# Performance work log

Hardware: AMD Instinct MI355X
Metric: run time of the kernel (lower is better)

## Reference

```python
import jax, jax.numpy as jnp
import numpy as np
import math

# tcnn HashGrid config (hard-coded in the torch module)
N_LEVELS = 16
N_FEATS = 2
LOG2_T = 19
T = 1 << LOG2_T            # 524288 entries per level
BASE_RES = 16
PER_LEVEL_SCALE = 1.4472692012786865
PRIMES = (1, 2654435761, 805459861)  # tcnn coherent spatial hash primes
N_POINTS = 1 << 20

# 8 trilinear corner offsets, [8, 3]
_OFFSETS = np.stack(np.meshgrid(*([np.arange(2)] * 3), indexing='ij'), -1).reshape(8, 3)


def _level_scale_res(level):
    # tcnn: grid_scale = base * s^l - 1 ; resolution = ceil(grid_scale) + 1
    scale = BASE_RES * (PER_LEVEL_SCALE ** level) - 1.0
    res = int(math.ceil(scale)) + 1
    return scale, res


def hashgrid_encode(coords, table):
    """coords: [..., 3] in [0,1]; table: [N_LEVELS, T, N_FEATS].
    Returns [..., N_LEVELS * N_FEATS]."""
    lead_shape = coords.shape[:-1]
    x = coords.reshape(-1, 3)                         # [N, 3]
    offs_i = jnp.asarray(_OFFSETS, dtype=jnp.uint32)  # [8, 3]
    offs_f = jnp.asarray(_OFFSETS, dtype=coords.dtype)
    feats = []
    for l in range(N_LEVELS):
        scale, res = _level_scale_res(l)
        pos = x * jnp.asarray(scale, x.dtype) + 0.5   # [N, 3]
        pf = jnp.floor(pos)
        w = pos - pf                                   # trilinear weights in [0,1)
        grid = pf.astype(jnp.uint32)                  # [N, 3]
        c = grid[None, :, :] + offs_i[:, None, :]     # [8, N, 3] corner coords
        if res ** 3 <= T:
            # dense (non-hashed) indexing for coarse levels
            cc = jnp.minimum(c, jnp.uint32(res - 1)).astype(jnp.int32)
            idx = cc[..., 0] + cc[..., 1] * res + cc[..., 2] * (res * res)
        else:
            # spatial hash: XOR of per-dim prime products, mod 2^19
            h = (c[..., 0] * jnp.uint32(PRIMES[0])
                 ^ c[..., 1] * jnp.uint32(PRIMES[1])
                 ^ c[..., 2] * jnp.uint32(PRIMES[2]))
            idx = (h & jnp.uint32(T - 1)).astype(jnp.int32)
        v = table[l][idx]                             # [8, N, F] gathered features
        # per-corner trilinear weight: prod over dims of (w or 1-w)
        wc = jnp.prod(jnp.where(offs_f[:, None, :] == 1.0, w[None], 1.0 - w[None]), axis=-1)  # [8, N]
        feats.append(jnp.einsum('kn,knf->nf', wc, v))  # [N, F]
    out = jnp.concatenate(feats, axis=-1)             # [N, 32]
    return out.reshape(*lead_shape, N_LEVELS * N_FEATS)


def setup_inputs() -> dict:
    key = jax.random.key(0)
    k1, k2 = jax.random.split(key)
    coords = jax.random.uniform(k1, (N_POINTS, 3), dtype=jnp.float32)
    # tcnn initializes hash table uniform in [-1e-4, 1e-4]
    table = jax.random.uniform(k2, (N_LEVELS, T, N_FEATS), dtype=jnp.float32,
                               minval=-1e-4, maxval=1e-4)
    return {"coords": coords, "table": table}


def reference(coords, table):
    return hashgrid_encode(coords, table)
```

## Files before the change

kernel.cpp:

```cpp
#include <hip/hip_runtime.h>
#include <math.h>

#define TBL   (1u << 19)
#define TMASK (TBL - 1u)
#define PRIME1 2654435761u
#define PRIME2 805459861u

#define N_DENSE  5u
#define N_HASH   11u

typedef float v2f __attribute__((ext_vector_type(2)));
typedef float v4f __attribute__((ext_vector_type(4)));

struct LevelParams {
    float    scale[16];
    unsigned res[16];
    unsigned dense[16];
};

__device__ __forceinline__ void corner_indices(
    float x, float y, float z, float s, unsigned res, unsigned dense,
    unsigned idx[8], float* wx, float* wy, float* wz)
{
    float px = __fadd_rn(__fmul_rn(x, s), 0.5f);
    float py = __fadd_rn(__fmul_rn(y, s), 0.5f);
    float pz = __fadd_rn(__fmul_rn(z, s), 0.5f);
    float fx = floorf(px), fy = floorf(py), fz = floorf(pz);
    *wx = px - fx; *wy = py - fy; *wz = pz - fz;
    unsigned gx = (unsigned)fx, gy = (unsigned)fy, gz = (unsigned)fz;

    if (dense) {
        const unsigned rm1 = res - 1u;
        unsigned cx0 = min(gx, rm1),   cx1 = min(gx + 1u, rm1);
        unsigned cy0 = min(gy, rm1),   cy1 = min(gy + 1u, rm1);
        unsigned cz0 = min(gz, rm1),   cz1 = min(gz + 1u, rm1);
        unsigned y0 = cy0 * res,       y1 = cy1 * res;
        unsigned z0 = cz0 * res * res, z1 = cz1 * res * res;
        idx[0] = cx0 + y0 + z0;  idx[1] = cx0 + y0 + z1;
        idx[2] = cx0 + y1 + z0;  idx[3] = cx0 + y1 + z1;
        idx[4] = cx1 + y0 + z0;  idx[5] = cx1 + y0 + z1;
        idx[6] = cx1 + y1 + z0;  idx[7] = cx1 + y1 + z1;
    } else {
        unsigned hx0 = gx,          hx1 = gx + 1u;
        unsigned hy0 = gy * PRIME1, hy1 = hy0 + PRIME1;
        unsigned hz0 = gz * PRIME2, hz1 = hz0 + PRIME2;
        idx[0] = (hx0 ^ hy0 ^ hz0) & TMASK;
        idx[1] = (hx0 ^ hy0 ^ hz1) & TMASK;
        idx[2] = (hx0 ^ hy1 ^ hz0) & TMASK;
        idx[3] = (hx0 ^ hy1 ^ hz1) & TMASK;
        idx[4] = (hx1 ^ hy0 ^ hz0) & TMASK;
        idx[5] = (hx1 ^ hy0 ^ hz1) & TMASK;
        idx[6] = (hx1 ^ hy1 ^ hz0) & TMASK;
        idx[7] = (hx1 ^ hy1 ^ hz1) & TMASK;
    }
}

__device__ __forceinline__ v2f interp_level(
    const v4f* __restrict__ tab4,
    float x, float y, float z, float s, unsigned res, unsigned dense)
{
    unsigned idx[8];
    float wx, wy, wz;
    corner_indices(x, y, z, s, res, dense, idx, &wx, &wy, &wz);

    float wx0 = 1.f - wx, wy0 = 1.f - wy, wz0 = 1.f - wz;
    float wyz00 = wy0 * wz0, wyz01 = wy0 * wz;
    float wyz10 = wy  * wz0, wyz11 = wy  * wz;
    float cw0[4] = { wx0 * wyz00, wx0 * wyz01, wx0 * wyz10, wx0 * wyz11 };
    float cw1[4] = { wx  * wyz00, wx  * wyz01, wx  * wyz10, wx  * wyz11 };

    float f0 = 0.f, f1 = 0.f;
    #pragma unroll
    for (int k = 0; k < 4; ++k) {
        unsigned i0 = idx[k], i1 = idx[k + 4];
        v4f q0 = tab4[i0 >> 1];
        v4f q1 = tab4[i1 >> 1];
        float a0 = (i0 & 1u) ? q0.z : q0.x;
        float b0 = (i0 & 1u) ? q0.w : q0.y;
        float a1 = (i1 & 1u) ? q1.z : q1.x;
        float b1 = (i1 & 1u) ? q1.w : q1.y;
        f0 = fmaf(cw0[k], a0, f0);
        f1 = fmaf(cw0[k], b0, f1);
        f0 = fmaf(cw1[k], a1, f0);
        f1 = fmaf(cw1[k], b1, f1);
    }
    v2f r; r.x = f0; r.y = f1;
    return r;
}

__global__ __launch_bounds__(256, 8) void pass_a(
    const float* __restrict__ coords,
    const float* __restrict__ table,
    v2f* __restrict__ ws,
    LevelParams lp, unsigned n)
{
    const unsigned li = blockIdx.y;
    const unsigned l  = li + N_DENSE;
    const unsigned p  = blockIdx.x * 256u + threadIdx.x;
    if (p >= n) return;

    const float x = coords[3ull * p + 0];
    const float y = coords[3ull * p + 1];
    const float z = coords[3ull * p + 2];

    const v4f* __restrict__ tab4 = (const v4f*)(table + (size_t)l * (2u * TBL));
    v2f r = interp_level(tab4, x, y, z, lp.scale[l], lp.res[l], 0u);
    ws[(size_t)li * n + p] = r;
}

__global__ __launch_bounds__(256, 4) void pass_b(
    const float* __restrict__ coords,
    const float* __restrict__ table,
    const v2f* __restrict__ ws,
    float* __restrict__ out,
    LevelParams lp, unsigned n)
{
    __shared__ float lds[256 * 33];
    const unsigned t  = threadIdx.x;
    const unsigned p0 = blockIdx.x * 256u;
    const unsigned p  = p0 + t;

    float x = 0.f, y = 0.f, z = 0.f;
    if (p < n) {
        x = coords[3ull * p + 0];
        y = coords[3ull * p + 1];
        z = coords[3ull * p + 2];
    }

    #pragma unroll
    for (int l = 0; l < (int)N_DENSE; ++l) {
        v2f r = {0.f, 0.f};
        if (p < n) {
            const v4f* __restrict__ tab4 =
                (const v4f*)(table + (size_t)l * (2u * TBL));
            r = interp_level(tab4, x, y, z, lp.scale[l], lp.res[l], 1u);
        }
        lds[t * 33u + 2u * l]      = r.x;
        lds[t * 33u + 2u * l + 1u] = r.y;
    }

    #pragma unroll
    for (int l = 0; l < (int)N_HASH; ++l) {
        v2f v = {0.f, 0.f};
        if (p < n) v = ws[(size_t)l * n + p];
        lds[t * 33u + 2u * (l + N_DENSE)]      = v.x;
        lds[t * 33u + 2u * (l + N_DENSE) + 1u] = v.y;
    }
    __syncthreads();

    v4f* __restrict__ out4 = (v4f*)out;
    const size_t base4  = (size_t)p0 * 8u;
    const size_t total4 = (size_t)n * 8u;
    #pragma unroll
    for (int i = 0; i < 8; ++i) {
        unsigned j = (unsigned)i * 256u + t;
        size_t o = base4 + j;
        if (o < total4) {
            unsigned pt = j >> 3, c = (j & 7u) * 4u;
            v4f q;
            q.x = lds[pt * 33u + c + 0u];
            q.y = lds[pt * 33u + c + 1u];
            q.z = lds[pt * 33u + c + 2u];
            q.w = lds[pt * 33u + c + 3u];
            __builtin_nontemporal_store(q, out4 + o);
        }
    }
}

__global__ __launch_bounds__(256, 4) void hashgrid_enc(
    const float* __restrict__ coords,
    const float* __restrict__ table,
    float* __restrict__ out,
    LevelParams lp, unsigned n)
{
    __shared__ float lds[256 * 33];
    const unsigned t = threadIdx.x;
    const unsigned p = blockIdx.x * 256u + t;

    float x = 0.f, y = 0.f, z = 0.f;
    if (p < n) {
        x = coords[3ull * p + 0];
        y = coords[3ull * p + 1];
        z = coords[3ull * p + 2];
    }

    #pragma unroll 2
    for (int l = 0; l < 16; ++l) {
        const v4f* __restrict__ tab4 = (const v4f*)(table + (size_t)l * (2u * TBL));
        v2f r = interp_level(tab4, x, y, z, lp.scale[l], lp.res[l], lp.dense[l]);
        lds[t * 33u + 2u * l]      = r.x;
        lds[t * 33u + 2u * l + 1u] = r.y;
    }
    __syncthreads();

    const size_t base  = (size_t)blockIdx.x * 8192u;
    const size_t total = (size_t)n * 32u;
    #pragma unroll
    for (int i = 0; i < 32; ++i) {
        size_t j = (size_t)i * 256u + t;
        size_t o = base + j;
        if (o < total)
            out[o] = lds[(unsigned)(j >> 5) * 33u + ((unsigned)j & 31u)];
    }
}

extern "C" void kernel_launch(void* const* d_in, const int* in_sizes, int n_in,
                              void* d_out, int out_size, void* d_ws, size_t ws_size,
                              hipStream_t stream) {
    (void)n_in; (void)out_size;
    const float* coords = (const float*)d_in[0];
    const float* table  = (const float*)d_in[1];
    float* out = (float*)d_out;

    LevelParams lp;
    for (int l = 0; l < 16; ++l) {
        double scale = 16.0 * pow(1.4472692012786865, (double)l) - 1.0;
        int res = (int)ceil(scale) + 1;
        lp.scale[l] = (float)scale;
        lp.res[l]   = (unsigned)res;
        long long r3 = (long long)res * res * res;
        lp.dense[l] = (r3 <= (long long)TBL) ? 1u : 0u;
    }

    unsigned n = (unsigned)(in_sizes[0] / 3);
    unsigned chunks = (n + 255u) / 256u;
    size_t ws_needed = (size_t)N_HASH * n * sizeof(v2f);

    if (ws_size >= ws_needed) {
        v2f* ws = (v2f*)d_ws;
        hipLaunchKernelGGL(pass_a, dim3(chunks, N_HASH), dim3(256), 0, stream,
                           coords, table, ws, lp, n);
        hipLaunchKernelGGL(pass_b, dim3(chunks), dim3(256), 0, stream,
                           coords, table, ws, out, lp, n);
    } else {
        hipLaunchKernelGGL(hashgrid_enc, dim3(chunks), dim3(256), 0, stream,
                           coords, table, out, lp, n);
    }
}
```

Measured before the change: 662.6 us.

## Split hash levels into interleaved pass and make final pass a pure transpose

The first pass now covers hashed levels 5-12 with the level interleaved fastest in the block index, so consecutive blocks share coordinates and spread their table traffic. A second pass covers levels 13-15 plus all dense levels. The final kernel only transposes the 16-level workspace to output through a halved LDS buffer, which allows higher occupancy. This adds an extra launch and more workspace traffic, since dense results now round-trip through memory, and it uses nontemporal loads and stores for the workspace.

```diff
diff --git a/kernel.cpp b/kernel.cpp
--- a/kernel.cpp
+++ b/kernel.cpp
@@ -88,15 +88,15 @@
     return r;
 }
 
-__global__ __launch_bounds__(256, 8) void pass_a(
+__global__ __launch_bounds__(256, 8) void pass_a1(
     const float* __restrict__ coords,
     const float* __restrict__ table,
     v2f* __restrict__ ws,
     LevelParams lp, unsigned n)
 {
-    const unsigned li = blockIdx.y;
-    const unsigned l  = li + N_DENSE;
-    const unsigned p  = blockIdx.x * 256u + threadIdx.x;
+    const unsigned b   = blockIdx.x;
+    const unsigned l   = 5u + (b & 7u);
+    const unsigned p   = (b >> 3) * 256u + threadIdx.x;
     if (p >= n) return;
 
     const float x = coords[3ull * p + 0];
@@ -105,64 +105,76 @@
 
     const v4f* __restrict__ tab4 = (const v4f*)(table + (size_t)l * (2u * TBL));
     v2f r = interp_level(tab4, x, y, z, lp.scale[l], lp.res[l], 0u);
-    ws[(size_t)li * n + p] = r;
-}
-
-__global__ __launch_bounds__(256, 4) void pass_b(
+    __builtin_nontemporal_store(r, ws + (size_t)l * n + p);
+}
+
+__global__ __launch_bounds__(256, 8) void pass_a2(
     const float* __restrict__ coords,
     const float* __restrict__ table,
+    v2f* __restrict__ ws,
+    LevelParams lp, unsigned n)
+{
+    const unsigned by = blockIdx.y;
+    const unsigned l  = (by < 3u) ? (13u + by) : (by - 3u);
+    const unsigned dn = (by < 3u) ? 0u : 1u;
+    const unsigned p  = blockIdx.x * 256u + threadIdx.x;
+    if (p >= n) return;
+
+    const float x = coords[3ull * p + 0];
+    const float y = coords[3ull * p + 1];
+    const float z = coords[3ull * p + 2];
+
+    const v4f* __restrict__ tab4 = (const v4f*)(table + (size_t)l * (2u * TBL));
+    v2f r = interp_level(tab4, x, y, z, lp.scale[l], lp.res[l], dn);
+    __builtin_nontemporal_store(r, ws + (size_t)l * n + p);
+}
+
+__global__ __launch_bounds__(256, 8) void pass_b(
     const v2f* __restrict__ ws,
-    float* __restrict__ out,
-    LevelParams lp, unsigned n)
-{
-    __shared__ float lds[256 * 33];
+    float* __restrict__ out, unsigned n)
+{
+    __shared__ float lds[128 * 33];
     const unsigned t  = threadIdx.x;
     const unsigned p0 = blockIdx.x * 256u;
     const unsigned p  = p0 + t;
 
-    float x = 0.f, y = 0.f, z = 0.f;
-    if (p < n) {
-        x = coords[3ull * p + 0];
-        y = coords[3ull * p + 1];
-        z = coords[3ull * p + 2];
-    }
-
-    #pragma unroll
-    for (int l = 0; l < (int)N_DENSE; ++l) {
-        v2f r = {0.f, 0.f};
-        if (p < n) {
-            const v4f* __restrict__ tab4 =
-                (const v4f*)(table + (size_t)l * (2u * TBL));
-            r = interp_level(tab4, x, y, z, lp.scale[l], lp.res[l], 1u);
+    v2f v[16];
+    #pragma unroll
+    for (int l = 0; l < 16; ++l) {
+        v2f q = {0.f, 0.f};
+        if (p < n) q = __builtin_nontemporal_load(ws + (size_t)l * n + p);
+        v[l] = q;
+    }
+
+    v4f* __restrict__ out4 = (v4f*)out;
+    const size_t total4 = (size_t)n * 8u;
+
+    #pragma unroll
+    for (int r = 0; r < 2; ++r) {
+        __syncthreads();
+        if ((t >> 7) == (unsigned)r) {
+            const unsigned tt = t & 127u;
+            #pragma unroll
+            for (int l = 0; l < 16; ++l) {
+                lds[tt * 33u + 2u * l]      = v[l].x;
+                lds[tt * 33u + 2u * l + 1u] = v[l].y;
+            }
         }
-        lds[t * 33u + 2u * l]      = r.x;
-        lds[t * 33u + 2u * l + 1u] = r.y;
-    }
-
-    #pragma unroll
-    for (int l = 0; l < (int)N_HASH; ++l) {
-        v2f v = {0.f, 0.f};
-        if (p < n) v = ws[(size_t)l * n + p];
-        lds[t * 33u + 2u * (l + N_DENSE)]      = v.x;
-        lds[t * 33u + 2u * (l + N_DENSE) + 1u] = v.y;
-    }
-    __syncthreads();
-
-    v4f* __restrict__ out4 = (v4f*)out;
-    const size_t base4  = (size_t)p0 * 8u;
-    const size_t total4 = (size_t)n * 8u;
-    #pragma unroll
-    for (int i = 0; i < 8; ++i) {
-        unsigned j = (unsigned)i * 256u + t;
-        size_t o = base4 + j;
-        if (o < total4) {
-            unsigned pt = j >> 3, c = (j & 7u) * 4u;
-            v4f q;
-            q.x = lds[pt * 33u + c + 0u];
-            q.y = lds[pt * 33u + c + 1u];
-            q.z = lds[pt * 33u + c + 2u];
-            q.w = lds[pt * 33u + c + 3u];
-            __builtin_nontemporal_store(q, out4 + o);
+        __syncthreads();
+        const size_t base4 = (size_t)(p0 + 128u * (unsigned)r) * 8u;
+        #pragma unroll
+        for (int i = 0; i < 4; ++i) {
+            unsigned j = (unsigned)i * 256u + t;
+            size_t o = base4 + j;
+            if (o < total4) {
+                unsigned pt = j >> 3, c = (j & 7u) * 4u;
+                v4f q;
+                q.x = lds[pt * 33u + c + 0u];
+                q.y = lds[pt * 33u + c + 1u];
+                q.z = lds[pt * 33u + c + 2u];
+                q.w = lds[pt * 33u + c + 3u];
+                __builtin_nontemporal_store(q, out4 + o);
+            }
         }
     }
 }
@@ -224,14 +236,16 @@
 
     unsigned n = (unsigned)(in_sizes[0] / 3);
     unsigned chunks = (n + 255u) / 256u;
-    size_t ws_needed = (size_t)N_HASH * n * sizeof(v2f);
+    size_t ws_needed = (size_t)16 * n * sizeof(v2f);
 
     if (ws_size >= ws_needed) {
         v2f* ws = (v2f*)d_ws;
-        hipLaunchKernelGGL(pass_a, dim3(chunks, N_HASH), dim3(256), 0, stream,
+        hipLaunchKernelGGL(pass_a1, dim3(chunks * 8u), dim3(256), 0, stream,
+                           coords, table, ws, lp, n);
+        hipLaunchKernelGGL(pass_a2, dim3(chunks, 8), dim3(256), 0, stream,
                            coords, table, ws, lp, n);
         hipLaunchKernelGGL(pass_b, dim3(chunks), dim3(256), 0, stream,
-                           coords, table, ws, out, lp, n);
+                           ws, out, n);
     } else {
         hipLaunchKernelGGL(hashgrid_enc, dim3(chunks), dim3(256), 0, stream,
                            coords, table, out, lp, n);
```

After: 659.1 us. Within noise of the previous version (-0.5%).
